# Optimization experiments

Measured on AMD Instinct MI355X. Metric: run time of the kernel, lower is better.

## Reference

```python
import jax, jax.numpy as jnp
import numpy as np

N = 7          # N_AGENTS (hardcoded in source)
H = 4          # n_heads
TOP_K = 3
EPS = 1e-5
NEG = -1.0e9


def _gat(x, W, a_src, a_dst, edge_mask):
    # x: (B,N,F), W: (F,H*Hd), a_src/a_dst: (H,Hd), edge_mask: (N,N)
    B = x.shape[0]
    Hd = a_src.shape[1]
    h = (x @ W).reshape(B, N, H, Hd)
    s_src = jnp.einsum('bnhd,hd->bnh', h, a_src)
    s_dst = jnp.einsum('bnhd,hd->bnh', h, a_dst)
    e = s_src[:, :, None, :] + s_dst[:, None, :, :]          # (B,N,N,H)
    e = jnp.where(e > 0, e, 0.2 * e)                          # LeakyReLU(0.2)
    m = edge_mask[None, :, :, None]
    e = e * m + (1.0 - m) * NEG
    if TOP_K < N:
        # k-th largest along axis=2 (ascending sort -> index N-TOP_K)
        thr = jnp.sort(e, axis=2)[:, :, N - TOP_K:N - TOP_K + 1, :]
        sm = (e >= thr).astype(e.dtype)
        e = e * sm + (1.0 - sm) * NEG
    alpha = jax.nn.softmax(e, axis=2)
    alpha = jnp.nan_to_num(alpha)
    out = jnp.einsum('bijh,bjhd->bihd', alpha, h).reshape(B, N, H * Hd)
    return out, alpha.mean(-1)


def _ln(x, w, b):
    mu = x.mean(-1, keepdims=True)
    var = ((x - mu) ** 2).mean(-1, keepdims=True)
    return (x - mu) / jnp.sqrt(var + EPS) * w + b


def _forward(node_feats, context, base_preds, regime_feats, edge_logits,
             W1, a_src1, a_dst1, W2, a_src2, a_dst2,
             ln1_w, ln1_b, ln2_w, ln2_b, skip_w, skip_b,
             base_w1, base_b1, base_w2, base_b2,
             reg_w1, reg_b1, reg_w2, reg_b2,
             gate_w1, gate_b1, gate_w2, gate_b2,
             res_w1, res_b1, res_w2, res_b2):
    B = node_feats.shape[0]
    eye = jnp.eye(N, dtype=edge_logits.dtype)
    edge_mask = jax.nn.sigmoid(edge_logits) * (1.0 - eye) + eye

    skip = node_feats @ skip_w + skip_b
    h1, _ = _gat(node_feats, W1, a_src1, a_dst1, edge_mask)
    h = jax.nn.relu(_ln(h1 + skip, ln1_w, ln1_b))
    h2, attn = _gat(h, W2, a_src2, a_dst2, edge_mask)
    h = jax.nn.relu(_ln(h2 + h, ln2_w, ln2_b))

    combined = jnp.concatenate([h.reshape(B, -1), context], axis=-1)
    w_base = jax.nn.softmax(jax.nn.relu(combined @ base_w1 + base_b1) @ base_w2 + base_b2, axis=-1)
    w_regime = jax.nn.softmax(jax.nn.relu(combined @ reg_w1 + reg_b1) @ reg_w2 + reg_b2, axis=-1)
    gate = jax.nn.sigmoid(jnp.tanh(regime_feats @ gate_w1 + gate_b1) @ gate_w2 + gate_b2)  # (B,1)
    weights = (1.0 - gate) * w_base + gate * w_regime
    pred = (weights * base_preds).sum(-1)
    residual = (jnp.tanh(combined @ res_w1 + res_b1) @ res_w2 + res_b2)[:, 0] * 0.05
    pred = jnp.maximum(pred + residual, 0.05)
    return pred, weights, gate, edge_mask, attn


def setup_inputs() -> dict:
    key = jax.random.key(0)
    B, F, C, HID, NB = 16384, 256, 128, 256, 2
    Hd = HID // H
    G = N * HID + C
    ks = iter(jax.random.split(key, 40))
    nrm = lambda shp, s: jax.random.normal(next(ks), shp, jnp.float32) * s
    d = {
        'node_feats': nrm((B, N, F), 1.0),
        'context': nrm((B, C), 1.0),
        'base_preds': jax.random.uniform(next(ks), (B, NB), jnp.float32),
        'regime_feats': nrm((B, 3), 1.0),
        'edge_logits': nrm((N, N), 0.1),
        'W1': nrm((F, HID), (2.0 / (F + HID)) ** 0.5),
        'a_src1': nrm((H, Hd), 0.1), 'a_dst1': nrm((H, Hd), 0.1),
        'W2': nrm((HID, HID), (1.0 / HID) ** 0.5),
        'a_src2': nrm((H, Hd), 0.1), 'a_dst2': nrm((H, Hd), 0.1),
        'ln1_w': jnp.ones((HID,), jnp.float32), 'ln1_b': jnp.zeros((HID,), jnp.float32),
        'ln2_w': jnp.ones((HID,), jnp.float32), 'ln2_b': jnp.zeros((HID,), jnp.float32),
        'skip_w': nrm((F, HID), (1.0 / F) ** 0.5), 'skip_b': jnp.zeros((HID,), jnp.float32),
        'base_w1': nrm((G, 32), (1.0 / G) ** 0.5), 'base_b1': jnp.zeros((32,), jnp.float32),
        'base_w2': nrm((32, NB), 0.1), 'base_b2': jnp.zeros((NB,), jnp.float32),
        'reg_w1': nrm((G, 32), (1.0 / G) ** 0.5), 'reg_b1': jnp.zeros((32,), jnp.float32),
        'reg_w2': nrm((32, NB), 0.1), 'reg_b2': jnp.zeros((NB,), jnp.float32),
        'gate_w1': nrm((3, 8), 0.5), 'gate_b1': jnp.zeros((8,), jnp.float32),
        'gate_w2': nrm((8, 1), 0.3), 'gate_b2': jnp.zeros((1,), jnp.float32),
        'res_w1': nrm((G, 16), (1.0 / G) ** 0.5), 'res_b1': jnp.zeros((16,), jnp.float32),
        'res_w2': nrm((16, 1), 0.2), 'res_b2': jnp.zeros((1,), jnp.float32),
    }
    return d


def reference(node_feats, context, base_preds, regime_feats, edge_logits,
              W1, a_src1, a_dst1, W2, a_src2, a_dst2,
              ln1_w, ln1_b, ln2_w, ln2_b, skip_w, skip_b,
              base_w1, base_b1, base_w2, base_b2,
              reg_w1, reg_b1, reg_w2, reg_b2,
              gate_w1, gate_b1, gate_w2, gate_b2,
              res_w1, res_b1, res_w2, res_b2):
    return _forward(node_feats, context, base_preds, regime_feats, edge_logits,
                    W1, a_src1, a_dst1, W2, a_src2, a_dst2,
                    ln1_w, ln1_b, ln2_w, ln2_b, skip_w, skip_b,
                    base_w1, base_b1, base_w2, base_b2,
                    reg_w1, reg_b1, reg_w2, reg_b2,
                    gate_w1, gate_b1, gate_w2, gate_b2,
                    res_w1, res_b1, res_w2, res_b2)
```

## Files before the change

### kernel.cpp

```cpp
#include <hip/hip_runtime.h>
#include <hip/hip_bf16.h>

typedef unsigned short u16;
typedef __attribute__((ext_vector_type(8))) short bfrag8;
typedef __attribute__((ext_vector_type(8))) unsigned short u16x8;
typedef __attribute__((ext_vector_type(4))) unsigned short u16x4;
typedef __attribute__((ext_vector_type(4))) float f32x4;

__device__ __forceinline__ float bf2f(u16 u) {
    union { unsigned int i; float f; } v; v.i = ((unsigned int)u) << 16; return v.f;
}
__device__ __forceinline__ u16 f2bf(float f) {
    union { __hip_bfloat16 h; u16 u; } cv;
    cv.h = __float2bfloat16(f);
    return cv.u;
}
__device__ __forceinline__ float fast_tanh(float x) {
    float e = __expf(2.f * x);
    return (e - 1.f) / (e + 1.f);
}

#define TILE_M 128
#define TILE_N 128
#define TILE_K 32

#define GLOAD_LDS16(g, l) \
    __builtin_amdgcn_global_load_lds( \
        (const __attribute__((address_space(1))) void*)(g), \
        (__attribute__((address_space(3))) void*)(l), 16, 0, 0)

template<int HAS_BIAS, int C_MODE, int NGUARD>
__global__ __launch_bounds__(256)
void gemm_k(const u16* __restrict__ A, const u16* __restrict__ Bt,
            const float* __restrict__ bias, void* __restrict__ Cp,
            int M, int N, int K, int lda, int ldc, int nt, int kchunk)
{
    __shared__ u16 As[TILE_M][TILE_K];
    __shared__ u16 Bs[TILE_N][TILE_K];

    const int nwg = gridDim.x;
    const int q = nwg >> 3, r = nwg & 7;
    const int xcd = blockIdx.x & 7, pos = blockIdx.x >> 3;
    const int wg = (xcd < r ? xcd * (q + 1) : r * (q + 1) + (xcd - r) * q) + pos;
    const int m0 = (wg / nt) * TILE_M;
    const int n0 = (wg % nt) * TILE_N;

    const int kc   = blockIdx.y;
    const int kbeg = kc * kchunk;
    const int kend = (kbeg + kchunk < K) ? kbeg + kchunk : K;

    const int t    = threadIdx.x;
    const int lane = t & 63;
    const int w    = t >> 6;
    const int wm   = (w >> 1) * 64;
    const int wn   = (w & 1) * 64;
    const int lr   = lane & 15;
    const int kg   = (lane >> 4) * 8;

    const int lrow = lane >> 2;
    const int lcol = (lane & 3) * 8;
    const u16* gA0 = A  + (size_t)(m0 + 32 * w + lrow) * lda + lcol;
    const u16* gA1 = gA0 + (size_t)16 * lda;
    const u16* gB0 = Bt + (size_t)(n0 + 32 * w + lrow) * K + lcol;
    const u16* gB1 = gB0 + (size_t)16 * K;
    char* lA0 = (char*)&As[0][0] + w * 2048;
    char* lA1 = lA0 + 1024;
    char* lB0 = (char*)&Bs[0][0] + w * 2048;
    char* lB1 = lB0 + 1024;

    f32x4 acc[4][4];
#pragma unroll
    for (int i = 0; i < 4; ++i)
#pragma unroll
        for (int j = 0; j < 4; ++j) acc[i][j] = (f32x4){0.f, 0.f, 0.f, 0.f};

    for (int k0 = kbeg; k0 < kend; k0 += TILE_K) {
        GLOAD_LDS16(gA0 + k0, lA0);
        GLOAD_LDS16(gA1 + k0, lA1);
        GLOAD_LDS16(gB0 + k0, lB0);
        GLOAD_LDS16(gB1 + k0, lB1);
        asm volatile("s_waitcnt vmcnt(0)" ::: "memory");
        __syncthreads();

        bfrag8 af[4], bfr[4];
#pragma unroll
        for (int mi = 0; mi < 4; ++mi) af[mi]  = *(const bfrag8*)&As[wm + mi * 16 + lr][kg];
#pragma unroll
        for (int ni = 0; ni < 4; ++ni) bfr[ni] = *(const bfrag8*)&Bs[wn + ni * 16 + lr][kg];
#pragma unroll
        for (int mi = 0; mi < 4; ++mi)
#pragma unroll
            for (int ni = 0; ni < 4; ++ni)
                acc[mi][ni] = __builtin_amdgcn_mfma_f32_16x16x32_bf16(af[mi], bfr[ni], acc[mi][ni], 0, 0, 0);

        __syncthreads();
    }

    float* Cf = (float*)Cp + (size_t)kc * M * ldc;
#pragma unroll
    for (int mi = 0; mi < 4; ++mi) {
#pragma unroll
        for (int ni = 0; ni < 4; ++ni) {
            int col = n0 + wn + ni * 16 + lr;
            if (!NGUARD || col < N) {
                int row = m0 + wm + mi * 16 + (lane >> 4) * 4;
                float bv = 0.f;
                if (HAS_BIAS && kc == 0) bv = bias[col];
#pragma unroll
                for (int rr = 0; rr < 4; ++rr) {
                    float v = acc[mi][ni][rr] + bv;
                    if (C_MODE == 0) ((u16*)Cp)[(size_t)(row + rr) * ldc + col] = f2bf(v);
                    else             Cf[(size_t)(row + rr) * ldc + col] = v;
                }
            }
        }
    }
}

__global__ __launch_bounds__(256)
void precast_k(const float* __restrict__ in, u16* __restrict__ out, int n8)
{
    int i = blockIdx.x * 256 + threadIdx.x;
    if (i >= n8) return;
    const float4* p = (const float4*)(in + (size_t)i * 8);
    float4 a = p[0], b = p[1];
    u16x8 v;
    v[0] = f2bf(a.x); v[1] = f2bf(a.y); v[2] = f2bf(a.z); v[3] = f2bf(a.w);
    v[4] = f2bf(b.x); v[5] = f2bf(b.y); v[6] = f2bf(b.z); v[7] = f2bf(b.w);
    *(u16x8*)(out + (size_t)i * 8) = v;
}

__global__ __launch_bounds__(256)
void score_k(const u16* __restrict__ hs, int ld,
             const float* __restrict__ a_src, const float* __restrict__ a_dst,
             float* __restrict__ scores, int Mrows)
{
    const int wid  = blockIdx.x * 4 + (threadIdx.x >> 6);
    const int lane = threadIdx.x & 63;
    if (wid >= Mrows) return;
    const u16* hp = hs + (size_t)wid * ld + lane * 4;
    u16x4 xv = *(const u16x4*)hp;
    float s1 = 0.f, s2 = 0.f;
#pragma unroll
    for (int k = 0; k < 4; ++k) {
        float x = bf2f(xv[k]);
        s1 = fmaf(x, a_src[lane * 4 + k], s1);
        s2 = fmaf(x, a_dst[lane * 4 + k], s2);
    }
#pragma unroll
    for (int off = 1; off < 16; off <<= 1) {
        s1 += __shfl_xor(s1, off);
        s2 += __shfl_xor(s2, off);
    }
    if ((lane & 15) == 0) {
        scores[(size_t)wid * 8 + (lane >> 4)] = s1;
        scores[(size_t)wid * 8 + 4 + (lane >> 4)] = s2;
    }
}

template<int WRITE_ATTN>
__global__ __launch_bounds__(256)
void alpha_k(const float* __restrict__ scores, const float* __restrict__ em2,
             float* __restrict__ alpha, float* __restrict__ attn_out)
{
    const int t = blockIdx.x * 256 + threadIdx.x;
    const int b = t >> 2;
    const int h = t & 3;

    float ssrc[7], sdst[7];
#pragma unroll
    for (int n = 0; n < 7; ++n) {
        ssrc[n] = scores[(size_t)(b * 7 + n) * 8 + h];
        sdst[n] = scores[(size_t)(b * 7 + n) * 8 + 4 + h];
    }

    float al[49];
#pragma unroll
    for (int i = 0; i < 7; ++i) {
        float e[7];
#pragma unroll
        for (int j = 0; j < 7; ++j) {
            float v = ssrc[i] + sdst[j];
            v = fmaxf(v, 0.2f * v);
            e[j] = fmaf(v, em2[(i * 7 + j) * 2], em2[(i * 7 + j) * 2 + 1]);
        }
        float a1 = -3e38f, b1 = -3e38f, c1 = -3e38f;
#pragma unroll
        for (int j = 0; j < 7; ++j) {
            float v = e[j];
            float t2 = fminf(a1, v); a1 = fmaxf(a1, v);
            float t3 = fminf(b1, t2); b1 = fmaxf(b1, t2);
            c1 = fmaxf(c1, t3);
        }
        float psum = 0.f;
        float p[7];
#pragma unroll
        for (int j = 0; j < 7; ++j) {
            float qv = (e[j] >= c1) ? __expf(e[j] - a1) : 0.f;
            p[j] = qv; psum += qv;
        }
        float inv = 1.f / psum;
#pragma unroll
        for (int j = 0; j < 7; ++j) al[i * 7 + j] = p[j] * inv;
    }

    float* ap = alpha + (size_t)t * 49;
#pragma unroll
    for (int j = 0; j < 49; ++j) ap[j] = al[j];

    if (WRITE_ATTN) {
#pragma unroll
        for (int j = 0; j < 49; ++j) {
            float m = al[j];
            m += __shfl_xor(m, 1);
            m += __shfl_xor(m, 2);
            if (h == 0) attn_out[(size_t)b * 49 + j] = 0.25f * m;
        }
    }
}

__global__ __launch_bounds__(256)
void gat_apply_k(const u16* __restrict__ hh, int ld_hh,
                 const u16* __restrict__ resid, int ld_res, int res_off,
                 const float* __restrict__ alpha,
                 const float* __restrict__ ln_w, const float* __restrict__ ln_b,
                 u16* __restrict__ outp, int out_bs)
{
    const int t = threadIdx.x;
    const int b = blockIdx.x * 4 + (t >> 6);
    const int l = t & 63;
    const int c = l * 4;
    const int h = l >> 4;
    const size_t rowbase = (size_t)b * 7;

    float hv[7][4];
#pragma unroll
    for (int n = 0; n < 7; ++n) {
        u16x4 qv = *(const u16x4*)&hh[(rowbase + n) * ld_hh + c];
#pragma unroll
        for (int k = 0; k < 4; ++k) hv[n][k] = bf2f(qv[k]);
    }

    const float* ap = alpha + ((size_t)b * 4 + h) * 49;
    float4 lw = *(const float4*)&ln_w[c];
    float4 lb = *(const float4*)&ln_b[c];

#pragma unroll
    for (int i = 0; i < 7; ++i) {
        float a0 = ap[i * 7 + 0], a1 = ap[i * 7 + 1], a2 = ap[i * 7 + 2],
              a3 = ap[i * 7 + 3], a4 = ap[i * 7 + 4], a5 = ap[i * 7 + 5],
              a6 = ap[i * 7 + 6];
        u16x4 rr = *(const u16x4*)&resid[(rowbase + i) * ld_res + res_off + c];
        float x[4];
#pragma unroll
        for (int k = 0; k < 4; ++k) {
            float pv = a0 * hv[0][k];
            pv = fmaf(a1, hv[1][k], pv);
            pv = fmaf(a2, hv[2][k], pv);
            pv = fmaf(a3, hv[3][k], pv);
            pv = fmaf(a4, hv[4][k], pv);
            pv = fmaf(a5, hv[5][k], pv);
            pv = fmaf(a6, hv[6][k], pv);
            x[k] = pv + bf2f(rr[k]);
        }
        float s1 = (x[0] + x[1]) + (x[2] + x[3]);
        float s2 = fmaf(x[0], x[0], x[1] * x[1]) + fmaf(x[2], x[2], x[3] * x[3]);
#pragma unroll
        for (int off = 32; off > 0; off >>= 1) {
            s1 += __shfl_xor(s1, off);
            s2 += __shfl_xor(s2, off);
        }
        float mu  = s1 * (1.f / 256.f);
        float var = fmaxf(s2 * (1.f / 256.f) - mu * mu, 0.f);
        float inv = rsqrtf(var + 1e-5f);
        u16x4 o;
        o[0] = f2bf(fmaxf((x[0] - mu) * inv * lw.x + lb.x, 0.f));
        o[1] = f2bf(fmaxf((x[1] - mu) * inv * lw.y + lb.y, 0.f));
        o[2] = f2bf(fmaxf((x[2] - mu) * inv * lw.z + lb.z, 0.f));
        o[3] = f2bf(fmaxf((x[3] - mu) * inv * lw.w + lb.w, 0.f));
        *(u16x4*)&outp[(size_t)b * out_bs + i * 256 + c] = o;
    }
}

__global__ __launch_bounds__(256)
void prep_k(const float* __restrict__ W1, const float* __restrict__ skip_w, const float* __restrict__ W2,
            const float* __restrict__ base_w1, const float* __restrict__ reg_w1, const float* __restrict__ res_w1,
            const float* __restrict__ skip_b, const float* __restrict__ base_b1, const float* __restrict__ reg_b1,
            const float* __restrict__ res_b1, const float* __restrict__ edge_logits,
            u16* __restrict__ Wt1, u16* __restrict__ Wt2, u16* __restrict__ Wt3,
            float* __restrict__ bias1, float* __restrict__ bias3,
            float* __restrict__ em2, float* __restrict__ em_out)
{
    int idx = blockIdx.x * 256 + threadIdx.x;
    if (idx < 512 * 256) {
        int n = idx >> 8, k = idx & 255;
        float v = (n < 256) ? W1[k * 256 + n] : skip_w[k * 256 + (n - 256)];
        Wt1[n * 256 + k] = f2bf(v); return;
    }
    idx -= 512 * 256;
    if (idx < 256 * 256) {
        int n = idx >> 8, k = idx & 255;
        Wt2[n * 256 + k] = f2bf(W2[k * 256 + n]); return;
    }
    idx -= 256 * 256;
    if (idx < 128 * 1920) {
        int n = idx / 1920, k = idx % 1920;
        float v = (n < 32) ? base_w1[k * 32 + n]
                : (n < 64) ? reg_w1[k * 32 + (n - 32)]
                : (n < 80) ? res_w1[k * 16 + (n - 64)] : 0.f;
        Wt3[n * 1920 + k] = f2bf(v); return;
    }
    idx -= 128 * 1920;
    if (idx < 512) { bias1[idx] = (idx < 256) ? 0.f : skip_b[idx - 256]; return; }
    idx -= 512;
    if (idx < 80) {
        bias3[idx] = (idx < 32) ? base_b1[idx] : (idx < 64) ? reg_b1[idx - 32] : res_b1[idx - 64];
        return;
    }
    idx -= 80;
    if (idx < 49) {
        int i = idx / 7, j = idx % 7;
        float s = 1.f / (1.f + __expf(-edge_logits[idx]));
        float m = (i == j) ? 1.f : s;
        em2[idx * 2] = m;
        em2[idx * 2 + 1] = (1.f - m) * (-1e9f);
        em_out[idx] = m;
    }
}

__global__ __launch_bounds__(256)
void ctx_k(const float* __restrict__ ctx, u16* __restrict__ comb)
{
    int idx = blockIdx.x * 256 + threadIdx.x;
    int b = idx >> 7, cc = idx & 127;
    comb[(size_t)b * 1920 + 1792 + cc] = f2bf(ctx[idx]);
}

__global__ __launch_bounds__(256)
void head_finish(const float* __restrict__ ho0, const float* __restrict__ ho1,
                 const float* __restrict__ bp, const float* __restrict__ rf,
                 const float* __restrict__ bw2, const float* __restrict__ bb2,
                 const float* __restrict__ rw2, const float* __restrict__ rb2,
                 const float* __restrict__ gw1, const float* __restrict__ gb1,
                 const float* __restrict__ gw2, const float* __restrict__ gb2,
                 const float* __restrict__ resw2, const float* __restrict__ resb2,
                 float* __restrict__ out_pred, float* __restrict__ out_w, float* __restrict__ out_gate, int B)
{
    int b = blockIdx.x * 256 + threadIdx.x;
    if (b >= B) return;
    const float* p0 = ho0 + (size_t)b * 80;
    const float* p1 = ho1 + (size_t)b * 80;
    float o[80];
#pragma unroll 16
    for (int k = 0; k < 80; ++k) o[k] = p0[k] + p1[k];

    float z0 = bb2[0], z1 = bb2[1];
#pragma unroll 8
    for (int k = 0; k < 32; ++k) { float v = fmaxf(o[k], 0.f); z0 += v * bw2[k * 2]; z1 += v * bw2[k * 2 + 1]; }
    float mz = fmaxf(z0, z1); float e0 = __expf(z0 - mz), e1 = __expf(z1 - mz); float inv = 1.f / (e0 + e1);
    float wb0 = e0 * inv, wb1 = e1 * inv;

    z0 = rb2[0]; z1 = rb2[1];
#pragma unroll 8
    for (int k = 0; k < 32; ++k) { float v = fmaxf(o[32 + k], 0.f); z0 += v * rw2[k * 2]; z1 += v * rw2[k * 2 + 1]; }
    mz = fmaxf(z0, z1); e0 = __expf(z0 - mz); e1 = __expf(z1 - mz); inv = 1.f / (e0 + e1);
    float wr0 = e0 * inv, wr1 = e1 * inv;

    float g = gb2[0];
#pragma unroll
    for (int j = 0; j < 8; ++j) {
        float a = gb1[j];
#pragma unroll
        for (int i = 0; i < 3; ++i) a += rf[(size_t)b * 3 + i] * gw1[i * 8 + j];
        g += fast_tanh(a) * gw2[j];
    }
    float gg = 1.f / (1.f + __expf(-g));
    float w0 = (1.f - gg) * wb0 + gg * wr0;
    float w1 = (1.f - gg) * wb1 + gg * wr1;
    float pred = w0 * bp[(size_t)b * 2] + w1 * bp[(size_t)b * 2 + 1];
    float r = resb2[0];
#pragma unroll 8
    for (int k = 0; k < 16; ++k) r += fast_tanh(o[64 + k]) * resw2[k];
    pred = fmaxf(pred + r * 0.05f, 0.05f);
    out_pred[b] = pred;
    out_w[(size_t)b * 2] = w0; out_w[(size_t)b * 2 + 1] = w1;
    out_gate[b] = gg;
}

extern "C" void kernel_launch(void* const* d_in, const int* in_sizes, int n_in,
                              void* d_out, int out_size, void* d_ws, size_t ws_size,
                              hipStream_t stream)
{
    const int B = in_sizes[1] / 128;
    const int Mbig = B * 7;

    const float* node_feats   = (const float*)d_in[0];
    const float* context      = (const float*)d_in[1];
    const float* base_preds   = (const float*)d_in[2];
    const float* regime_feats = (const float*)d_in[3];
    const float* edge_logits  = (const float*)d_in[4];
    const float* W1      = (const float*)d_in[5];
    const float* a_src1  = (const float*)d_in[6];
    const float* a_dst1  = (const float*)d_in[7];
    const float* W2      = (const float*)d_in[8];
    const float* a_src2  = (const float*)d_in[9];
    const float* a_dst2  = (const float*)d_in[10];
    const float* ln1_w   = (const float*)d_in[11];
    const float* ln1_b   = (const float*)d_in[12];
    const float* ln2_w   = (const float*)d_in[13];
    const float* ln2_b   = (const float*)d_in[14];
    const float* skip_w  = (const float*)d_in[15];
    const float* skip_b  = (const float*)d_in[16];
    const float* base_w1 = (const float*)d_in[17];
    const float* base_b1 = (const float*)d_in[18];
    const float* base_w2 = (const float*)d_in[19];
    const float* base_b2 = (const float*)d_in[20];
    const float* reg_w1  = (const float*)d_in[21];
    const float* reg_b1  = (const float*)d_in[22];
    const float* reg_w2  = (const float*)d_in[23];
    const float* reg_b2  = (const float*)d_in[24];
    const float* gate_w1 = (const float*)d_in[25];
    const float* gate_b1 = (const float*)d_in[26];
    const float* gate_w2 = (const float*)d_in[27];
    const float* gate_b2 = (const float*)d_in[28];
    const float* res_w1  = (const float*)d_in[29];
    const float* res_b1  = (const float*)d_in[30];
    const float* res_w2  = (const float*)d_in[31];
    const float* res_b2  = (const float*)d_in[32];

    char* ws = (char*)d_ws;
    size_t off = 0;
    u16* hs1 = (u16*)(ws + off);
    u16* hh2 = (u16*)(ws + off);
    off += (size_t)Mbig * 512 * 2;
    u16* hbuf = (u16*)(ws + off);  off += (size_t)Mbig * 256 * 2;
    u16* comb = (u16*)(ws + off);  off += (size_t)B * 1920 * 2;
    u16* nf_bf = comb;
    float* headout = (float*)(ws + off); off += (size_t)2 * B * 80 * 4;
    u16* Wt1 = (u16*)(ws + off); off += 512 * 256 * 2;
    u16* Wt2 = (u16*)(ws + off); off += 256 * 256 * 2;
    u16* Wt3 = (u16*)(ws + off); off += (size_t)128 * 1920 * 2;
    float* bias1 = (float*)(ws + off); off += 512 * 4;
    float* bias3 = (float*)(ws + off); off += 128 * 4;
    float* em2   = (float*)(ws + off); off += 128 * 4;
    float* scoresb = (float*)(ws + off); off += (size_t)Mbig * 8 * 4;
    float* alphab  = (float*)(ws + off); off += (size_t)B * 4 * 49 * 4;

    float* out_pred = (float*)d_out;
    float* out_w    = out_pred + B;
    float* out_gate = out_pred + 3 * (size_t)B;
    float* out_em   = out_pred + 4 * (size_t)B;
    float* out_attn = out_pred + 4 * (size_t)B + 49;

    const int B4blocks = (B * 4) / 256;

    {
        int n8 = Mbig * 256 / 8;
        precast_k<<<dim3((n8 + 255) / 256), dim3(256), 0, stream>>>(node_feats, nf_bf, n8);
    }

    prep_k<<<dim3(1731), dim3(256), 0, stream>>>(W1, skip_w, W2, base_w1, reg_w1, res_w1,
        skip_b, base_b1, reg_b1, res_b1, edge_logits, Wt1, Wt2, Wt3, bias1, bias3, em2, out_em);

    gemm_k<1, 0, 0><<<dim3((Mbig / 128) * 4, 1), dim3(256), 0, stream>>>(
        nf_bf, Wt1, bias1, (void*)hs1, Mbig, 512, 256, 256, 512, 4, 256);

    score_k<<<dim3(Mbig / 4), dim3(256), 0, stream>>>(hs1, 512, a_src1, a_dst1, scoresb, Mbig);

    alpha_k<0><<<dim3(B4blocks), dim3(256), 0, stream>>>(scoresb, em2, alphab, (float*)nullptr);

    gat_apply_k<<<dim3(B / 4), dim3(256), 0, stream>>>(
        hs1, 512, hs1, 512, 256, alphab, ln1_w, ln1_b, hbuf, 1792);

    gemm_k<0, 0, 0><<<dim3((Mbig / 128) * 2, 1), dim3(256), 0, stream>>>(
        hbuf, Wt2, (const float*)nullptr, (void*)hh2, Mbig, 256, 256, 256, 256, 2, 256);

    score_k<<<dim3(Mbig / 4), dim3(256), 0, stream>>>(hh2, 256, a_src2, a_dst2, scoresb, Mbig);

    alpha_k<1><<<dim3(B4blocks), dim3(256), 0, stream>>>(scoresb, em2, alphab, out_attn);

    gat_apply_k<<<dim3(B / 4), dim3(256), 0, stream>>>(
        hh2, 256, hbuf, 256, 0, alphab, ln2_w, ln2_b, comb, 1920);

    ctx_k<<<dim3(B * 128 / 256), dim3(256), 0, stream>>>(context, comb);

    gemm_k<1, 1, 1><<<dim3(B / 128, 2), dim3(256), 0, stream>>>(
        comb, Wt3, bias3, (void*)headout, B, 80, 1920, 1920, 80, 1, 960);

    head_finish<<<dim3((B + 255) / 256), dim3(256), 0, stream>>>(
        headout, headout + (size_t)B * 80, base_preds, regime_feats, base_w2, base_b2, reg_w2, reg_b2,
        gate_w1, gate_b1, gate_w2, gate_b2, res_w2, res_b2, out_pred, out_w, out_gate, B);
}
```

Baseline: 312.8 us.

## Double-buffer GEMM LDS tiles and raise head GEMM split-K to four

The GEMM kernel now uses two LDS buffers and issues the global-to-LDS loads for the next K tile before computing the current one. It waits with vmcnt(4) so those loads overlap the MFMA work. Separately, the head GEMM is split into four K chunks instead of two for more parallelism, and head_finish sums four partial outputs. This doubles LDS use per block, which may lower occupancy, and adds partial-sum traffic.

```diff
diff --git a/kernel.cpp b/kernel.cpp
--- a/kernel.cpp
+++ b/kernel.cpp
@@ -35,8 +35,8 @@
             const float* __restrict__ bias, void* __restrict__ Cp,
             int M, int N, int K, int lda, int ldc, int nt, int kchunk)
 {
-    __shared__ u16 As[TILE_M][TILE_K];
-    __shared__ u16 Bs[TILE_N][TILE_K];
+    __shared__ u16 As[2][TILE_M][TILE_K];
+    __shared__ u16 Bs[2][TILE_N][TILE_K];
 
     const int nwg = gridDim.x;
     const int q = nwg >> 3, r = nwg & 7;
@@ -63,10 +63,8 @@
     const u16* gA1 = gA0 + (size_t)16 * lda;
     const u16* gB0 = Bt + (size_t)(n0 + 32 * w + lrow) * K + lcol;
     const u16* gB1 = gB0 + (size_t)16 * K;
-    char* lA0 = (char*)&As[0][0] + w * 2048;
-    char* lA1 = lA0 + 1024;
-    char* lB0 = (char*)&Bs[0][0] + w * 2048;
-    char* lB1 = lB0 + 1024;
+    char* lA = (char*)&As[0][0][0] + w * 2048;
+    char* lB = (char*)&Bs[0][0][0] + w * 2048;
 
     f32x4 acc[4][4];
 #pragma unroll
@@ -74,19 +72,30 @@
 #pragma unroll
         for (int j = 0; j < 4; ++j) acc[i][j] = (f32x4){0.f, 0.f, 0.f, 0.f};
 
+#define ISSUE(bufo, k0v) { \
+        GLOAD_LDS16(gA0 + (k0v), lA + (bufo)); \
+        GLOAD_LDS16(gA1 + (k0v), lA + 1024 + (bufo)); \
+        GLOAD_LDS16(gB0 + (k0v), lB + (bufo)); \
+        GLOAD_LDS16(gB1 + (k0v), lB + 1024 + (bufo)); \
+    }
+
+    ISSUE(0, kbeg)
+    int buf = 0;
     for (int k0 = kbeg; k0 < kend; k0 += TILE_K) {
-        GLOAD_LDS16(gA0 + k0, lA0);
-        GLOAD_LDS16(gA1 + k0, lA1);
-        GLOAD_LDS16(gB0 + k0, lB0);
-        GLOAD_LDS16(gB1 + k0, lB1);
-        asm volatile("s_waitcnt vmcnt(0)" ::: "memory");
+        const bool more = (k0 + TILE_K) < kend;
+        if (more) {
+            ISSUE((buf ^ 1) * 8192, k0 + TILE_K);
+            asm volatile("s_waitcnt vmcnt(4)" ::: "memory");
+        } else {
+            asm volatile("s_waitcnt vmcnt(0)" ::: "memory");
+        }
         __syncthreads();
 
         bfrag8 af[4], bfr[4];
 #pragma unroll
-        for (int mi = 0; mi < 4; ++mi) af[mi]  = *(const bfrag8*)&As[wm + mi * 16 + lr][kg];
-#pragma unroll
-        for (int ni = 0; ni < 4; ++ni) bfr[ni] = *(const bfrag8*)&Bs[wn + ni * 16 + lr][kg];
+        for (int mi = 0; mi < 4; ++mi) af[mi]  = *(const bfrag8*)&As[buf][wm + mi * 16 + lr][kg];
+#pragma unroll
+        for (int ni = 0; ni < 4; ++ni) bfr[ni] = *(const bfrag8*)&Bs[buf][wn + ni * 16 + lr][kg];
 #pragma unroll
         for (int mi = 0; mi < 4; ++mi)
 #pragma unroll
@@ -94,7 +103,9 @@
                 acc[mi][ni] = __builtin_amdgcn_mfma_f32_16x16x32_bf16(af[mi], bfr[ni], acc[mi][ni], 0, 0, 0);
 
         __syncthreads();
-    }
+        buf ^= 1;
+    }
+#undef ISSUE
 
     float* Cf = (float*)Cp + (size_t)kc * M * ldc;
 #pragma unroll
@@ -337,7 +348,7 @@
 }
 
 __global__ __launch_bounds__(256)
-void head_finish(const float* __restrict__ ho0, const float* __restrict__ ho1,
+void head_finish(const float* __restrict__ ho,
                  const float* __restrict__ bp, const float* __restrict__ rf,
                  const float* __restrict__ bw2, const float* __restrict__ bb2,
                  const float* __restrict__ rw2, const float* __restrict__ rb2,
@@ -348,11 +359,12 @@
 {
     int b = blockIdx.x * 256 + threadIdx.x;
     if (b >= B) return;
-    const float* p0 = ho0 + (size_t)b * 80;
-    const float* p1 = ho1 + (size_t)b * 80;
+    const size_t ss = (size_t)B * 80;
+    const float* p0 = ho + (size_t)b * 80;
     float o[80];
 #pragma unroll 16
-    for (int k = 0; k < 80; ++k) o[k] = p0[k] + p1[k];
+    for (int k = 0; k < 80; ++k)
+        o[k] = (p0[k] + p0[ss + k]) + (p0[2 * ss + k] + p0[3 * ss + k]);
 
     float z0 = bb2[0], z1 = bb2[1];
 #pragma unroll 8
@@ -436,7 +448,7 @@
     u16* hbuf = (u16*)(ws + off);  off += (size_t)Mbig * 256 * 2;
     u16* comb = (u16*)(ws + off);  off += (size_t)B * 1920 * 2;
     u16* nf_bf = comb;
-    float* headout = (float*)(ws + off); off += (size_t)2 * B * 80 * 4;
+    float* headout = (float*)(ws + off); off += (size_t)4 * B * 80 * 4;
     u16* Wt1 = (u16*)(ws + off); off += 512 * 256 * 2;
     u16* Wt2 = (u16*)(ws + off); off += 256 * 256 * 2;
     u16* Wt3 = (u16*)(ws + off); off += (size_t)128 * 1920 * 2;
@@ -484,10 +496,10 @@
 
     ctx_k<<<dim3(B * 128 / 256), dim3(256), 0, stream>>>(context, comb);
 
-    gemm_k<1, 1, 1><<<dim3(B / 128, 2), dim3(256), 0, stream>>>(
-        comb, Wt3, bias3, (void*)headout, B, 80, 1920, 1920, 80, 1, 960);
+    gemm_k<1, 1, 1><<<dim3(B / 128, 4), dim3(256), 0, stream>>>(
+        comb, Wt3, bias3, (void*)headout, B, 80, 1920, 1920, 80, 1, 480);
 
     head_finish<<<dim3((B + 255) / 256), dim3(256), 0, stream>>>(
-        headout, headout + (size_t)B * 80, base_preds, regime_feats, base_w2, base_b2, reg_w2, reg_b2,
+        headout, base_preds, regime_feats, base_w2, base_b2, reg_w2, reg_b2,
         gate_w1, gate_b1, gate_w2, gate_b2, res_w2, res_b2, out_pred, out_w, out_gate, B);
 }
```

After: 301.2 us. -3.7%, faster.
